# Optimization experiments

Hardware: AMD Instinct MI355X
Metric: run time of the kernel (lower is better)

## Reference

```python
import jax, jax.numpy as jnp
import numpy as np

N = 100000   # nodes
E = 1600000  # edges
IN = 32
HID = 64
OUT = 1

def setup_inputs() -> dict:
    key = jax.random.key(0)
    ks = jax.random.split(key, 16)
    x = jax.random.normal(ks[0], (N, IN), jnp.float32)
    edge_index = jax.random.randint(ks[1], (2, E), 0, N, dtype=jnp.int32)
    def lin(k, fi, fo):
        return jax.random.normal(k, (fi, fo), jnp.float32) / np.sqrt(fi)
    # SAGEConv params per layer: Wn/bn for aggregated neighbors (lin_l), Wr for root (lin_r, no bias)
    Wn0 = lin(ks[2], IN, HID);  bn0 = jnp.zeros((HID,), jnp.float32); Wr0 = lin(ks[3], IN, HID)
    Wn1 = lin(ks[4], HID, HID); bn1 = jnp.zeros((HID,), jnp.float32); Wr1 = lin(ks[5], HID, HID)
    Wn2 = lin(ks[6], HID, HID); bn2 = jnp.zeros((HID,), jnp.float32); Wr2 = lin(ks[7], HID, HID)
    # predictor MLP
    Wp1 = lin(ks[8], HID, HID); bp1 = jnp.zeros((HID,), jnp.float32)
    Wp2 = lin(ks[9], HID, OUT); bp2 = jnp.zeros((OUT,), jnp.float32)
    return dict(x=x, edge_index=edge_index,
                Wn0=Wn0, bn0=bn0, Wr0=Wr0,
                Wn1=Wn1, bn1=bn1, Wr1=Wr1,
                Wn2=Wn2, bn2=bn2, Wr2=Wr2,
                Wp1=Wp1, bp1=bp1, Wp2=Wp2, bp2=bp2)

def reference(x, edge_index, Wn0, bn0, Wr0, Wn1, bn1, Wr1, Wn2, bn2, Wr2, Wp1, bp1, Wp2, bp2):
    src, dst = edge_index[0], edge_index[1]
    n = x.shape[0]
    # mean-aggregation normalization (nodes with no in-edges get 0, as in PyG)
    cnt = jax.ops.segment_sum(jnp.ones(src.shape, x.dtype), dst, num_segments=n)
    inv = jnp.where(cnt > 0, 1.0 / jnp.maximum(cnt, 1.0), 0.0)[:, None]

    def sage(h, Wn, bn, Wr):
        agg = jax.ops.segment_sum(h[src], dst, num_segments=n) * inv  # [N, d]
        return agg @ Wn + bn + h @ Wr

    h = jax.nn.relu(sage(x, Wn0, bn0, Wr0))
    h = jax.nn.relu(sage(h, Wn1, bn1, Wr1))
    h = sage(h, Wn2, bn2, Wr2)  # no activation after last GNN layer
    h = jax.nn.relu(h @ Wp1 + bp1)
    return jax.nn.sigmoid(h @ Wp2 + bp2)
```

## Files before the change

kernel.cpp:

```cpp
#include <hip/hip_runtime.h>
#include <math.h>

#define NN 100000
#define EE 1600000
#define HID 64
#define BKT 391
#define SLAB 5504
#define SLAB_IT ((SLAB + 255) / 256)
#define CHUNK 4096
#define NWG ((EE + CHUNK - 1) / CHUNK)
#define TB (NN / 16)

typedef _Float16 f16;
typedef _Float16 f16x2 __attribute__((ext_vector_type(2)));

__device__ __forceinline__ f16x2 u2h(unsigned u) { return __builtin_bit_cast(f16x2, u); }
__device__ __forceinline__ unsigned h2u(f16x2 h) { return __builtin_bit_cast(unsigned, h); }

#if defined(__has_builtin) && __has_builtin(__builtin_amdgcn_fdot2)
__device__ __forceinline__ float dot2(f16x2 a, f16x2 b, float c) {
    return __builtin_amdgcn_fdot2(a, b, c, false);
}
#else
__device__ __forceinline__ float dot2(f16x2 a, f16x2 b, float c) {
    c = fmaf((float)a.x, (float)b.x, c);
    return fmaf((float)a.y, (float)b.y, c);
}
#endif


#if defined(__has_builtin)
#if __has_builtin(__builtin_amdgcn_cvt_pk_f32_fp8) && __has_builtin(__builtin_amdgcn_cvt_pk_fp8_f32)
#define HW_FP8 1
#endif
#endif

#ifndef HW_FP8
__device__ __forceinline__ float dec_e4m3(unsigned b) {
    unsigned s = b >> 7, e = (b >> 3) & 0xF, m = b & 7;
    float v;
    if (e == 0) v = (float)m * 0.001953125f;
    else v = (1.f + (float)m * 0.125f) * exp2f((float)((int)e - 7));
    return s ? -v : v;
}
__device__ __forceinline__ unsigned char enc_e4m3(float x) {
    unsigned s = (__builtin_bit_cast(unsigned, x) >> 31) << 7;
    float a = fabsf(x);
    if (!(a < 464.f)) return (unsigned char)(s | 0x7E);
    int e; float m = frexpf(a, &e);
    int E = e - 1;
    unsigned bits;
    if (E < -6) {
        int n = (int)rintf(a * 512.f);
        bits = (n > 7) ? 0x08u : (unsigned)n;
    } else {
        int n = (int)rintf((2.f * m - 1.f) * 8.f);
        if (n == 8) { n = 0; E += 1; }
        if (E > 8) return (unsigned char)(s | 0x7E);
        bits = ((unsigned)(E + 7) << 3) | (unsigned)n;
    }
    return (unsigned char)(s | bits);
}
#endif

__device__ __forceinline__ void acc_fp8(unsigned v, float& a0, float& a1,
                                        float& a2, float& a3) {
#ifdef HW_FP8
    auto lo = __builtin_amdgcn_cvt_pk_f32_fp8((int)v, false);
    auto hi = __builtin_amdgcn_cvt_pk_f32_fp8((int)v, true);
    a0 += lo[0]; a1 += lo[1]; a2 += hi[0]; a3 += hi[1];
#else
    a0 += dec_e4m3(v & 0xFFu);         a1 += dec_e4m3((v >> 8) & 0xFFu);
    a2 += dec_e4m3((v >> 16) & 0xFFu); a3 += dec_e4m3(v >> 24);
#endif
}

__device__ __forceinline__ unsigned char enc_fp8(float x) {
#ifdef HW_FP8
    return (unsigned char)(__builtin_amdgcn_cvt_pk_fp8_f32(x, x, 0, false) & 0xFF);
#else
    return enc_e4m3(x);
#endif
}


__global__ void mt_kernel(const int* __restrict__ src, const int* __restrict__ dst,
                          int* __restrict__ bfill, unsigned* __restrict__ pairs,
                          const float* __restrict__ h,
                          const float* __restrict__ Wn, const float* __restrict__ bn,
                          const float* __restrict__ Wr,
                          unsigned char* __restrict__ hn8, f16* __restrict__ hrb,
                          const float* __restrict__ Wn1, const float* __restrict__ Wr1,
                          const float* __restrict__ Wn2, const float* __restrict__ Wr2,
                          const float* __restrict__ Wp1, unsigned* __restrict__ w16) {
    __shared__ int lc[BKT];
    __shared__ int lbase[BKT];
    int t = threadIdx.x;

    if (blockIdx.x < NWG) {
        for (int b = t; b < BKT; b += 256) lc[b] = 0;
        __syncthreads();
        int base = blockIdx.x * CHUNK;
        int myd[CHUNK / 256];
        int myr[CHUNK / 256];
#pragma unroll
        for (int j = 0; j < CHUNK / 256; ++j) {
            int i = base + j * 256 + t;
            myd[j] = (i < EE) ? dst[i] : -1;
            myr[j] = (myd[j] >= 0) ? atomicAdd(&lc[myd[j] >> 8], 1) : 0;
        }
        __syncthreads();
        for (int b = t; b < BKT; b += 256) {
            int c = lc[b];
            if (c) {
                int ofs = atomicAdd(&bfill[b], c);
                if (ofs + c > SLAB) ofs = SLAB - c;
                lbase[b] = b * SLAB + ofs;
            }
        }
        __syncthreads();
#pragma unroll
        for (int j = 0; j < CHUNK / 256; ++j) {
            int i = base + j * 256 + t;
            if (myd[j] >= 0) {
                int b = myd[j] >> 8;
                pairs[lbase[b] + myr[j]] = (unsigned)src[i] | ((unsigned)(myd[j] & 255) << 24);
            }
        }
        return;
    }

    int bb = blockIdx.x - NWG;

    if (bb < 40) {
        int id = bb * 256 + t;
        int mat = id >> 11;
        int p = (id >> 6) & 31;
        int j = id & 63;
        const float* W = (mat == 0) ? Wn1 : (mat == 1) ? Wr1 :
                         (mat == 2) ? Wn2 : (mat == 3) ? Wr2 : Wp1;
        f16x2 v;
        v.x = (f16)W[(2 * p) * HID + j];
        v.y = (f16)W[(2 * p + 1) * HID + j];
        w16[id] = h2u(v);
    }

    int lane = t & 63;
    int wid = (bb * 256 + t) >> 6;
    int m0 = __builtin_amdgcn_readfirstlane(wid << 2);
    const float* h0 = h + (size_t)m0 * 32;

    float an0 = 0.f, an1 = 0.f, an2 = 0.f, an3 = 0.f;
    float ar0 = 0.f, ar1 = 0.f, ar2 = 0.f, ar3 = 0.f;
#pragma unroll
    for (int k = 0; k < 32; ++k) {
        float wn = Wn[k * HID + lane];
        float wr = Wr[k * HID + lane];
        float hk0 = h0[k], hk1 = h0[32 + k], hk2 = h0[64 + k], hk3 = h0[96 + k];
        an0 = fmaf(hk0, wn, an0); ar0 = fmaf(hk0, wr, ar0);
        an1 = fmaf(hk1, wn, an1); ar1 = fmaf(hk1, wr, ar1);
        an2 = fmaf(hk2, wn, an2); ar2 = fmaf(hk2, wr, ar2);
        an3 = fmaf(hk3, wn, an3); ar3 = fmaf(hk3, wr, ar3);
    }
    float b = bn[lane];
    size_t o8 = (size_t)m0 * HID + lane;
    hn8[o8] = enc_fp8(an0);
    hn8[o8 + HID] = enc_fp8(an1);
    hn8[o8 + 2 * HID] = enc_fp8(an2);
    hn8[o8 + 3 * HID] = enc_fp8(an3);
    size_t o = (size_t)m0 * HID + lane;
    hrb[o] = (f16)(ar0 + b); hrb[o + HID] = (f16)(ar1 + b);
    hrb[o + 2 * HID] = (f16)(ar2 + b); hrb[o + 3 * HID] = (f16)(ar3 + b);
}


__global__ void build_kernel(const unsigned* __restrict__ pairs,
                             const int* __restrict__ bfill,
                             int* __restrict__ rs, int* __restrict__ re,
                             float* __restrict__ inv, int* __restrict__ col) {
    __shared__ int ncnt[256];
    __shared__ int nexcl[256];
    int b = blockIdx.x;
    int t = threadIdx.x;
    int s0 = b * SLAB;
    int ce = bfill[b]; if (ce > SLAB) ce = SLAB;
    ncnt[t] = 0;
    __syncthreads();
    unsigned mypk[SLAB_IT];
    int myr[SLAB_IT];
#pragma unroll
    for (int j = 0; j < SLAB_IT; ++j) {
        int e = j * 256 + t;
        if (e < ce) {
            unsigned pk = pairs[s0 + e];
            mypk[j] = pk;
            myr[j] = atomicAdd(&ncnt[pk >> 24], 1);
        }
    }
    __syncthreads();
    int c = ncnt[t];
    int c4 = (c + 3) & ~3;
    nexcl[t] = c4;
    __syncthreads();
    for (int off = 1; off < 256; off <<= 1) {
        int u = (t >= off) ? nexcl[t - off] : 0;
        __syncthreads();
        nexcl[t] += u;
        __syncthreads();
    }
    int excl = nexcl[t] - c4;
    int node = (b << 8) + t;
    if (node < NN) {
        int start = s0 + excl; if (start > s0 + SLAB) start = s0 + SLAB;
        int end = start + c;   if (end > s0 + SLAB) end = s0 + SLAB;
        rs[node] = start;
        re[node] = end;
        inv[node] = (c > 0) ? (1.0f / (float)c) : 0.0f;
    }
    __syncthreads();
    ncnt[t] = excl;
    __syncthreads();
#pragma unroll
    for (int j = 0; j < SLAB_IT; ++j) {
        int e = j * 256 + t;
        if (e < ce) {
            unsigned pk = mypk[j];
            int idx = s0 + ncnt[pk >> 24] + myr[j];
            if (idx < s0 + SLAB) col[idx] = (int)(pk & 0xFFFFFFu);
        }
    }
    for (int k = c; k < c4; ++k) {
        int idx = s0 + excl + k;
        if (idx < s0 + SLAB) col[idx] = NN;
    }
}


__device__ __forceinline__ void qgather8(const unsigned* __restrict__ rp,
                                         const int* __restrict__ col,
                                         int e, int en, int en4, int fl,
                                         float& a0, float& a1, float& a2, float& a3) {
    while (e + 8 <= en4) {
        int4 ca = *(const int4*)(col + e);
        int4 cb = *(const int4*)(col + e + 4);
        unsigned v0 = rp[(size_t)ca.x * 16 + fl];
        unsigned v1 = rp[(size_t)ca.y * 16 + fl];
        unsigned v2 = rp[(size_t)ca.z * 16 + fl];
        unsigned v3 = rp[(size_t)ca.w * 16 + fl];
        unsigned v4 = rp[(size_t)cb.x * 16 + fl];
        unsigned v5 = rp[(size_t)cb.y * 16 + fl];
        unsigned v6 = rp[(size_t)cb.z * 16 + fl];
        unsigned v7 = rp[(size_t)cb.w * 16 + fl];
        acc_fp8(v0, a0, a1, a2, a3);
        acc_fp8(v1, a0, a1, a2, a3);
        acc_fp8(v2, a0, a1, a2, a3);
        acc_fp8(v3, a0, a1, a2, a3);
        acc_fp8(v4, a0, a1, a2, a3);
        acc_fp8(v5, a0, a1, a2, a3);
        acc_fp8(v6, a0, a1, a2, a3);
        acc_fp8(v7, a0, a1, a2, a3);
        e += 8;
    }
    if (e + 4 <= en4) {
        int4 ca = *(const int4*)(col + e);
        unsigned v0 = rp[(size_t)ca.x * 16 + fl];
        unsigned v1 = rp[(size_t)ca.y * 16 + fl];
        unsigned v2 = rp[(size_t)ca.z * 16 + fl];
        unsigned v3 = rp[(size_t)ca.w * 16 + fl];
        acc_fp8(v0, a0, a1, a2, a3);
        acc_fp8(v1, a0, a1, a2, a3);
        acc_fp8(v2, a0, a1, a2, a3);
        acc_fp8(v3, a0, a1, a2, a3);
        e += 4;
    }
    while (e < en) {
        unsigned v = rp[(size_t)col[e] * 16 + fl];
        acc_fp8(v, a0, a1, a2, a3);
        ++e;
    }
}


__global__ void gt_kernel(const unsigned char* __restrict__ An8,
                          const int* __restrict__ rs, const int* __restrict__ re,
                          const int* __restrict__ col, const float* __restrict__ inv,
                          f16* C,
                          const unsigned* __restrict__ Wn16, const float* __restrict__ bn,
                          const unsigned* __restrict__ Wr16,
                          unsigned char* __restrict__ Aout8) {
    __shared__ uint4 hsh[128];
    int t = threadIdx.x;
    int lane = t & 63;
    int wv = t >> 6;
    int wid = (blockIdx.x * blockDim.x + t) >> 6;
    int m0 = wid << 2;
    int m = m0 + (lane >> 4);
    int fl = lane & 15;

    int e = rs[m], en = re[m];
    int en4 = e + ((en - e + 3) & ~3);
    int bnd = ((m >> 8) + 1) * SLAB;
    if (en4 > bnd) en4 = bnd;

    float a0 = 0.f, a1 = 0.f, a2 = 0.f, a3 = 0.f;
    qgather8((const unsigned*)An8, col, e, en, en4, fl, a0, a1, a2, a3);

    float iv = inv[m];
    uint2 cur = ((const uint2*)C)[(size_t)m * 16 + fl];
    f16x2 q0 = u2h(cur.x), q1 = u2h(cur.y);
    f16x2 hA, hB;
    hA.x = (f16)fmaxf(fmaf(a0, iv, (float)q0.x), 0.f);
    hA.y = (f16)fmaxf(fmaf(a1, iv, (float)q0.y), 0.f);
    hB.x = (f16)fmaxf(fmaf(a2, iv, (float)q1.x), 0.f);
    hB.y = (f16)fmaxf(fmaf(a3, iv, (float)q1.y), 0.f);

    uint2 hv; hv.x = h2u(hA); hv.y = h2u(hB);
    ((uint2*)hsh)[wv * 64 + (lane >> 4) * 16 + fl] = hv;

    float an[4] = {0.f, 0.f, 0.f, 0.f};
    float ar[4] = {0.f, 0.f, 0.f, 0.f};
#pragma unroll
    for (int j = 0; j < 8; ++j) {
        f16x2 wn0 = u2h(Wn16[(4 * j) * HID + lane]);
        f16x2 wn1 = u2h(Wn16[(4 * j + 1) * HID + lane]);
        f16x2 wn2 = u2h(Wn16[(4 * j + 2) * HID + lane]);
        f16x2 wn3 = u2h(Wn16[(4 * j + 3) * HID + lane]);
        f16x2 wr0 = u2h(Wr16[(4 * j) * HID + lane]);
        f16x2 wr1 = u2h(Wr16[(4 * j + 1) * HID + lane]);
        f16x2 wr2 = u2h(Wr16[(4 * j + 2) * HID + lane]);
        f16x2 wr3 = u2h(Wr16[(4 * j + 3) * HID + lane]);
#pragma unroll
        for (int n = 0; n < 4; ++n) {
            uint4 d = hsh[wv * 32 + n * 8 + j];
            an[n] = dot2(u2h(d.x), wn0, an[n]);
            an[n] = dot2(u2h(d.y), wn1, an[n]);
            an[n] = dot2(u2h(d.z), wn2, an[n]);
            an[n] = dot2(u2h(d.w), wn3, an[n]);
            ar[n] = dot2(u2h(d.x), wr0, ar[n]);
            ar[n] = dot2(u2h(d.y), wr1, ar[n]);
            ar[n] = dot2(u2h(d.z), wr2, ar[n]);
            ar[n] = dot2(u2h(d.w), wr3, ar[n]);
        }
    }
    float b = bn[lane];
    size_t o8 = (size_t)m0 * HID + lane;
    size_t o = (size_t)m0 * HID + lane;
#pragma unroll
    for (int n = 0; n < 4; ++n) {
        Aout8[o8 + n * HID] = enc_fp8(an[n]);
        C[o + n * HID] = (f16)(ar[n] + b);
    }
}


__global__ void gh_kernel(const unsigned char* __restrict__ An8,
                          const int* __restrict__ rs, const int* __restrict__ re,
                          const int* __restrict__ col, const float* __restrict__ inv,
                          const f16* __restrict__ C,
                          const unsigned* __restrict__ Wp116, const float* __restrict__ bp1,
                          const float* __restrict__ Wp2, const float* __restrict__ bp2,
                          float* __restrict__ out) {
    __shared__ uint4 hsh[128];
    int t = threadIdx.x;
    int lane = t & 63;
    int wv = t >> 6;
    int wid = (blockIdx.x * blockDim.x + t) >> 6;
    int m0 = wid << 2;
    int m = m0 + (lane >> 4);
    int fl = lane & 15;

    int e = rs[m], en = re[m];
    int en4 = e + ((en - e + 3) & ~3);
    int bnd = ((m >> 8) + 1) * SLAB;
    if (en4 > bnd) en4 = bnd;

    float a0 = 0.f, a1 = 0.f, a2 = 0.f, a3 = 0.f;
    qgather8((const unsigned*)An8, col, e, en, en4, fl, a0, a1, a2, a3);

    float iv = inv[m];
    uint2 cur = ((const uint2*)C)[(size_t)m * 16 + fl];
    f16x2 q0 = u2h(cur.x), q1 = u2h(cur.y);
    f16x2 hA, hB;
    hA.x = (f16)fmaf(a0, iv, (float)q0.x);
    hA.y = (f16)fmaf(a1, iv, (float)q0.y);
    hB.x = (f16)fmaf(a2, iv, (float)q1.x);
    hB.y = (f16)fmaf(a3, iv, (float)q1.y);

    uint2 hv; hv.x = h2u(hA); hv.y = h2u(hB);
    ((uint2*)hsh)[wv * 64 + (lane >> 4) * 16 + fl] = hv;

    float tn[4] = {0.f, 0.f, 0.f, 0.f};
#pragma unroll
    for (int j = 0; j < 8; ++j) {
        f16x2 wp0 = u2h(Wp116[(4 * j) * HID + lane]);
        f16x2 wp1 = u2h(Wp116[(4 * j + 1) * HID + lane]);
        f16x2 wp2 = u2h(Wp116[(4 * j + 2) * HID + lane]);
        f16x2 wp3 = u2h(Wp116[(4 * j + 3) * HID + lane]);
#pragma unroll
        for (int n = 0; n < 4; ++n) {
            uint4 d = hsh[wv * 32 + n * 8 + j];
            tn[n] = dot2(u2h(d.x), wp0, tn[n]);
            tn[n] = dot2(u2h(d.y), wp1, tn[n]);
            tn[n] = dot2(u2h(d.z), wp2, tn[n]);
            tn[n] = dot2(u2h(d.w), wp3, tn[n]);
        }
    }
    float b = bp1[lane], w2v = Wp2[lane];
    float r0 = fmaxf(tn[0] + b, 0.f) * w2v;
    float r1 = fmaxf(tn[1] + b, 0.f) * w2v;
    float r2 = fmaxf(tn[2] + b, 0.f) * w2v;
    float r3 = fmaxf(tn[3] + b, 0.f) * w2v;
#pragma unroll
    for (int off = 32; off > 0; off >>= 1) {
        r0 += __shfl_xor(r0, off);
        r1 += __shfl_xor(r1, off);
        r2 += __shfl_xor(r2, off);
        r3 += __shfl_xor(r3, off);
    }
    if (lane == 0) {
        float bb = bp2[0];
        out[m0]     = 1.f / (1.f + expf(-(r0 + bb)));
        out[m0 + 1] = 1.f / (1.f + expf(-(r1 + bb)));
        out[m0 + 2] = 1.f / (1.f + expf(-(r2 + bb)));
        out[m0 + 3] = 1.f / (1.f + expf(-(r3 + bb)));
    }
}

extern "C" void kernel_launch(void* const* d_in, const int* in_sizes, int n_in,
                              void* d_out, int out_size, void* d_ws, size_t ws_size,
                              hipStream_t stream) {
    const float* x   = (const float*)d_in[0];
    const int* eidx  = (const int*)d_in[1];
    const float* Wn0 = (const float*)d_in[2];
    const float* bn0 = (const float*)d_in[3];
    const float* Wr0 = (const float*)d_in[4];
    const float* Wn1 = (const float*)d_in[5];
    const float* bn1 = (const float*)d_in[6];
    const float* Wr1 = (const float*)d_in[7];
    const float* Wn2 = (const float*)d_in[8];
    const float* bn2 = (const float*)d_in[9];
    const float* Wr2 = (const float*)d_in[10];
    const float* Wp1 = (const float*)d_in[11];
    const float* bp1 = (const float*)d_in[12];
    const float* Wp2 = (const float*)d_in[13];
    const float* bp2 = (const float*)d_in[14];
    float* out = (float*)d_out;

    const int* src = eidx;
    const int* dst = eidx + EE;

    char* w = (char*)d_ws;
    size_t off = 0;
    auto carve = [&](size_t bytes) -> void* {
        void* p = w + off;
        off = (off + bytes + 255) & ~(size_t)255;
        return p;
    };
    int*   rsA    = (int*)carve((size_t)NN * 4);
    int*   reA    = (int*)carve((size_t)NN * 4);
    float* inv    = (float*)carve((size_t)NN * 4);
    int*   col    = (int*)carve((size_t)BKT * SLAB * 4);
    int*   bfill  = (int*)carve((size_t)BKT * 4);
    unsigned* w16 = (unsigned*)carve((size_t)5 * 2048 * 4);
    unsigned char* A0 = (unsigned char*)carve((size_t)(NN + 1) * HID);
    unsigned char* A1 = (unsigned char*)carve((size_t)(NN + 1) * HID);
    f16*   C      = (f16*)carve((size_t)NN * HID * 2);
    unsigned* pairs = (unsigned*)carve((size_t)BKT * SLAB * 4);
    (void)ws_size;

    unsigned* Wn1_16 = w16;
    unsigned* Wr1_16 = w16 + 2048;
    unsigned* Wn2_16 = w16 + 4096;
    unsigned* Wr2_16 = w16 + 6144;
    unsigned* Wp1_16 = w16 + 8192;

    hipMemsetAsync(bfill, 0, (size_t)BKT * 4, stream);
    hipMemsetAsync(A0 + (size_t)NN * HID, 0, HID, stream);
    hipMemsetAsync(A1 + (size_t)NN * HID, 0, HID, stream);

    mt_kernel<<<NWG + TB, 256, 0, stream>>>(src, dst, bfill, pairs,
                                            x, Wn0, bn0, Wr0, A0, C,
                                            Wn1, Wr1, Wn2, Wr2, Wp1, w16);
    build_kernel<<<BKT, 256, 0, stream>>>(pairs, bfill, rsA, reA, inv, col);

    gt_kernel<<<TB, 256, 0, stream>>>(A0, rsA, reA, col, inv, C, Wn1_16, bn1, Wr1_16, A1);
    gt_kernel<<<TB, 256, 0, stream>>>(A1, rsA, reA, col, inv, C, Wn2_16, bn2, Wr2_16, A0);
    gh_kernel<<<TB, 256, 0, stream>>>(A0, rsA, reA, col, inv, C, Wp1_16, bp1, Wp2, bp2, out);
}
```

Before: 244.2 us.

## Widen gather loads to 8 bytes per lane and split edges across half-groups

The neighbor gather in the hidden and head kernels now has each lane load 8 fp8 features (uint2) rather than 4. The 16 lanes for a node split into two groups of 8 that take alternating edges, and their partial sums are combined with an xor shuffle. Root features are read as uint4 and only half the lanes write to shared memory. Separately, the first-layer transform in mt_kernel now handles 8 nodes per wave instead of 4, which halves its block count and raises register use.

```diff
diff --git a/kernel.cpp b/kernel.cpp
--- a/kernel.cpp
+++ b/kernel.cpp
@@ -10,6 +10,7 @@
 #define CHUNK 4096
 #define NWG ((EE + CHUNK - 1) / CHUNK)
 #define TB (NN / 16)
+#define TBM (NN / 32)
 
 typedef _Float16 f16;
 typedef _Float16 f16x2 __attribute__((ext_vector_type(2)));
@@ -147,30 +148,30 @@
 
     int lane = t & 63;
     int wid = (bb * 256 + t) >> 6;
-    int m0 = __builtin_amdgcn_readfirstlane(wid << 2);
+    int m0 = __builtin_amdgcn_readfirstlane(wid << 3);
     const float* h0 = h + (size_t)m0 * 32;
 
-    float an0 = 0.f, an1 = 0.f, an2 = 0.f, an3 = 0.f;
-    float ar0 = 0.f, ar1 = 0.f, ar2 = 0.f, ar3 = 0.f;
+    float an[8] = {0.f, 0.f, 0.f, 0.f, 0.f, 0.f, 0.f, 0.f};
+    float ar[8] = {0.f, 0.f, 0.f, 0.f, 0.f, 0.f, 0.f, 0.f};
 #pragma unroll
     for (int k = 0; k < 32; ++k) {
         float wn = Wn[k * HID + lane];
         float wr = Wr[k * HID + lane];
-        float hk0 = h0[k], hk1 = h0[32 + k], hk2 = h0[64 + k], hk3 = h0[96 + k];
-        an0 = fmaf(hk0, wn, an0); ar0 = fmaf(hk0, wr, ar0);
-        an1 = fmaf(hk1, wn, an1); ar1 = fmaf(hk1, wr, ar1);
-        an2 = fmaf(hk2, wn, an2); ar2 = fmaf(hk2, wr, ar2);
-        an3 = fmaf(hk3, wn, an3); ar3 = fmaf(hk3, wr, ar3);
+#pragma unroll
+        for (int n = 0; n < 8; ++n) {
+            float hk = h0[n * 32 + k];
+            an[n] = fmaf(hk, wn, an[n]);
+            ar[n] = fmaf(hk, wr, ar[n]);
+        }
     }
     float b = bn[lane];
     size_t o8 = (size_t)m0 * HID + lane;
-    hn8[o8] = enc_fp8(an0);
-    hn8[o8 + HID] = enc_fp8(an1);
-    hn8[o8 + 2 * HID] = enc_fp8(an2);
-    hn8[o8 + 3 * HID] = enc_fp8(an3);
     size_t o = (size_t)m0 * HID + lane;
-    hrb[o] = (f16)(ar0 + b); hrb[o + HID] = (f16)(ar1 + b);
-    hrb[o + 2 * HID] = (f16)(ar2 + b); hrb[o + 3 * HID] = (f16)(ar3 + b);
+#pragma unroll
+    for (int n = 0; n < 8; ++n) {
+        hn8[o8 + n * HID] = enc_fp8(an[n]);
+        hrb[o + n * HID] = (f16)(ar[n] + b);
+    }
 }
 
 
@@ -236,46 +237,50 @@
 }
 
 
-__device__ __forceinline__ void qgather8(const unsigned* __restrict__ rp,
-                                         const int* __restrict__ col,
-                                         int e, int en, int en4, int fl,
-                                         float& a0, float& a1, float& a2, float& a3) {
+__device__ __forceinline__ void acc8(uint2 v, float& a0, float& a1, float& a2,
+                                     float& a3, float& a4, float& a5, float& a6,
+                                     float& a7) {
+    acc_fp8(v.x, a0, a1, a2, a3);
+    acc_fp8(v.y, a4, a5, a6, a7);
+}
+
+__device__ __forceinline__ void qgp(const uint2* __restrict__ rp2,
+                                    const int* __restrict__ col,
+                                    int e, int en, int en4, int ff, int el,
+                                    float& a0, float& a1, float& a2, float& a3,
+                                    float& a4, float& a5, float& a6, float& a7) {
     while (e + 8 <= en4) {
         int4 ca = *(const int4*)(col + e);
         int4 cb = *(const int4*)(col + e + 4);
-        unsigned v0 = rp[(size_t)ca.x * 16 + fl];
-        unsigned v1 = rp[(size_t)ca.y * 16 + fl];
-        unsigned v2 = rp[(size_t)ca.z * 16 + fl];
-        unsigned v3 = rp[(size_t)ca.w * 16 + fl];
-        unsigned v4 = rp[(size_t)cb.x * 16 + fl];
-        unsigned v5 = rp[(size_t)cb.y * 16 + fl];
-        unsigned v6 = rp[(size_t)cb.z * 16 + fl];
-        unsigned v7 = rp[(size_t)cb.w * 16 + fl];
-        acc_fp8(v0, a0, a1, a2, a3);
-        acc_fp8(v1, a0, a1, a2, a3);
-        acc_fp8(v2, a0, a1, a2, a3);
-        acc_fp8(v3, a0, a1, a2, a3);
-        acc_fp8(v4, a0, a1, a2, a3);
-        acc_fp8(v5, a0, a1, a2, a3);
-        acc_fp8(v6, a0, a1, a2, a3);
-        acc_fp8(v7, a0, a1, a2, a3);
+        int c0 = el ? ca.y : ca.x;
+        int c1 = el ? ca.w : ca.z;
+        int c2 = el ? cb.y : cb.x;
+        int c3 = el ? cb.w : cb.z;
+        uint2 v0 = rp2[(size_t)c0 * 8 + ff];
+        uint2 v1 = rp2[(size_t)c1 * 8 + ff];
+        uint2 v2 = rp2[(size_t)c2 * 8 + ff];
+        uint2 v3 = rp2[(size_t)c3 * 8 + ff];
+        acc8(v0, a0, a1, a2, a3, a4, a5, a6, a7);
+        acc8(v1, a0, a1, a2, a3, a4, a5, a6, a7);
+        acc8(v2, a0, a1, a2, a3, a4, a5, a6, a7);
+        acc8(v3, a0, a1, a2, a3, a4, a5, a6, a7);
         e += 8;
     }
     if (e + 4 <= en4) {
         int4 ca = *(const int4*)(col + e);
-        unsigned v0 = rp[(size_t)ca.x * 16 + fl];
-        unsigned v1 = rp[(size_t)ca.y * 16 + fl];
-        unsigned v2 = rp[(size_t)ca.z * 16 + fl];
-        unsigned v3 = rp[(size_t)ca.w * 16 + fl];
-        acc_fp8(v0, a0, a1, a2, a3);
-        acc_fp8(v1, a0, a1, a2, a3);
-        acc_fp8(v2, a0, a1, a2, a3);
-        acc_fp8(v3, a0, a1, a2, a3);
+        int c0 = el ? ca.y : ca.x;
+        int c1 = el ? ca.w : ca.z;
+        uint2 v0 = rp2[(size_t)c0 * 8 + ff];
+        uint2 v1 = rp2[(size_t)c1 * 8 + ff];
+        acc8(v0, a0, a1, a2, a3, a4, a5, a6, a7);
+        acc8(v1, a0, a1, a2, a3, a4, a5, a6, a7);
         e += 4;
     }
     while (e < en) {
-        unsigned v = rp[(size_t)col[e] * 16 + fl];
-        acc_fp8(v, a0, a1, a2, a3);
+        if (!el) {
+            uint2 v = rp2[(size_t)col[e] * 8 + ff];
+            acc8(v, a0, a1, a2, a3, a4, a5, a6, a7);
+        }
         ++e;
     }
 }
@@ -295,7 +300,8 @@
     int wid = (blockIdx.x * blockDim.x + t) >> 6;
     int m0 = wid << 2;
     int m = m0 + (lane >> 4);
-    int fl = lane & 15;
+    int ff = lane & 7;
+    int el = (lane >> 3) & 1;
 
     int e = rs[m], en = re[m];
     int en4 = e + ((en - e + 3) & ~3);
@@ -303,19 +309,30 @@
     if (en4 > bnd) en4 = bnd;
 
     float a0 = 0.f, a1 = 0.f, a2 = 0.f, a3 = 0.f;
-    qgather8((const unsigned*)An8, col, e, en, en4, fl, a0, a1, a2, a3);
+    float a4 = 0.f, a5 = 0.f, a6 = 0.f, a7 = 0.f;
+    qgp((const uint2*)An8, col, e, en, en4, ff, el, a0, a1, a2, a3, a4, a5, a6, a7);
+
+    a0 += __shfl_xor(a0, 8); a1 += __shfl_xor(a1, 8);
+    a2 += __shfl_xor(a2, 8); a3 += __shfl_xor(a3, 8);
+    a4 += __shfl_xor(a4, 8); a5 += __shfl_xor(a5, 8);
+    a6 += __shfl_xor(a6, 8); a7 += __shfl_xor(a7, 8);
 
     float iv = inv[m];
-    uint2 cur = ((const uint2*)C)[(size_t)m * 16 + fl];
-    f16x2 q0 = u2h(cur.x), q1 = u2h(cur.y);
-    f16x2 hA, hB;
-    hA.x = (f16)fmaxf(fmaf(a0, iv, (float)q0.x), 0.f);
-    hA.y = (f16)fmaxf(fmaf(a1, iv, (float)q0.y), 0.f);
-    hB.x = (f16)fmaxf(fmaf(a2, iv, (float)q1.x), 0.f);
-    hB.y = (f16)fmaxf(fmaf(a3, iv, (float)q1.y), 0.f);
-
-    uint2 hv; hv.x = h2u(hA); hv.y = h2u(hB);
-    ((uint2*)hsh)[wv * 64 + (lane >> 4) * 16 + fl] = hv;
+    uint4 cur = ((const uint4*)C)[(size_t)m * 8 + ff];
+    f16x2 q0 = u2h(cur.x), q1 = u2h(cur.y), q2 = u2h(cur.z), q3 = u2h(cur.w);
+    f16x2 p0, p1, p2, p3;
+    p0.x = (f16)fmaxf(fmaf(a0, iv, (float)q0.x), 0.f);
+    p0.y = (f16)fmaxf(fmaf(a1, iv, (float)q0.y), 0.f);
+    p1.x = (f16)fmaxf(fmaf(a2, iv, (float)q1.x), 0.f);
+    p1.y = (f16)fmaxf(fmaf(a3, iv, (float)q1.y), 0.f);
+    p2.x = (f16)fmaxf(fmaf(a4, iv, (float)q2.x), 0.f);
+    p2.y = (f16)fmaxf(fmaf(a5, iv, (float)q2.y), 0.f);
+    p3.x = (f16)fmaxf(fmaf(a6, iv, (float)q3.x), 0.f);
+    p3.y = (f16)fmaxf(fmaf(a7, iv, (float)q3.y), 0.f);
+
+    uint4 hv4;
+    hv4.x = h2u(p0); hv4.y = h2u(p1); hv4.z = h2u(p2); hv4.w = h2u(p3);
+    if (!(lane & 8)) hsh[wv * 32 + (lane >> 4) * 8 + ff] = hv4;
 
     float an[4] = {0.f, 0.f, 0.f, 0.f};
     float ar[4] = {0.f, 0.f, 0.f, 0.f};
@@ -367,7 +384,8 @@
     int wid = (blockIdx.x * blockDim.x + t) >> 6;
     int m0 = wid << 2;
     int m = m0 + (lane >> 4);
-    int fl = lane & 15;
+    int ff = lane & 7;
+    int el = (lane >> 3) & 1;
 
     int e = rs[m], en = re[m];
     int en4 = e + ((en - e + 3) & ~3);
@@ -375,19 +393,30 @@
     if (en4 > bnd) en4 = bnd;
 
     float a0 = 0.f, a1 = 0.f, a2 = 0.f, a3 = 0.f;
-    qgather8((const unsigned*)An8, col, e, en, en4, fl, a0, a1, a2, a3);
+    float a4 = 0.f, a5 = 0.f, a6 = 0.f, a7 = 0.f;
+    qgp((const uint2*)An8, col, e, en, en4, ff, el, a0, a1, a2, a3, a4, a5, a6, a7);
+
+    a0 += __shfl_xor(a0, 8); a1 += __shfl_xor(a1, 8);
+    a2 += __shfl_xor(a2, 8); a3 += __shfl_xor(a3, 8);
+    a4 += __shfl_xor(a4, 8); a5 += __shfl_xor(a5, 8);
+    a6 += __shfl_xor(a6, 8); a7 += __shfl_xor(a7, 8);
 
     float iv = inv[m];
-    uint2 cur = ((const uint2*)C)[(size_t)m * 16 + fl];
-    f16x2 q0 = u2h(cur.x), q1 = u2h(cur.y);
-    f16x2 hA, hB;
-    hA.x = (f16)fmaf(a0, iv, (float)q0.x);
-    hA.y = (f16)fmaf(a1, iv, (float)q0.y);
-    hB.x = (f16)fmaf(a2, iv, (float)q1.x);
-    hB.y = (f16)fmaf(a3, iv, (float)q1.y);
-
-    uint2 hv; hv.x = h2u(hA); hv.y = h2u(hB);
-    ((uint2*)hsh)[wv * 64 + (lane >> 4) * 16 + fl] = hv;
+    uint4 cur = ((const uint4*)C)[(size_t)m * 8 + ff];
+    f16x2 q0 = u2h(cur.x), q1 = u2h(cur.y), q2 = u2h(cur.z), q3 = u2h(cur.w);
+    f16x2 p0, p1, p2, p3;
+    p0.x = (f16)fmaf(a0, iv, (float)q0.x);
+    p0.y = (f16)fmaf(a1, iv, (float)q0.y);
+    p1.x = (f16)fmaf(a2, iv, (float)q1.x);
+    p1.y = (f16)fmaf(a3, iv, (float)q1.y);
+    p2.x = (f16)fmaf(a4, iv, (float)q2.x);
+    p2.y = (f16)fmaf(a5, iv, (float)q2.y);
+    p3.x = (f16)fmaf(a6, iv, (float)q3.x);
+    p3.y = (f16)fmaf(a7, iv, (float)q3.y);
+
+    uint4 hv4;
+    hv4.x = h2u(p0); hv4.y = h2u(p1); hv4.z = h2u(p2); hv4.w = h2u(p3);
+    if (!(lane & 8)) hsh[wv * 32 + (lane >> 4) * 8 + ff] = hv4;
 
     float tn[4] = {0.f, 0.f, 0.f, 0.f};
 #pragma unroll
@@ -478,9 +507,9 @@
     hipMemsetAsync(A0 + (size_t)NN * HID, 0, HID, stream);
     hipMemsetAsync(A1 + (size_t)NN * HID, 0, HID, stream);
 
-    mt_kernel<<<NWG + TB, 256, 0, stream>>>(src, dst, bfill, pairs,
-                                            x, Wn0, bn0, Wr0, A0, C,
-                                            Wn1, Wr1, Wn2, Wr2, Wp1, w16);
+    mt_kernel<<<NWG + TBM, 256, 0, stream>>>(src, dst, bfill, pairs,
+                                             x, Wn0, bn0, Wr0, A0, C,
+                                             Wn1, Wr1, Wn2, Wr2, Wp1, w16);
     build_kernel<<<BKT, 256, 0, stream>>>(pairs, bfill, rsA, reA, inv, col);
 
     gt_kernel<<<TB, 256, 0, stream>>>(A0, rsA, reA, col, inv, C, Wn1_16, bn1, Wr1_16, A1);
```

Result: no change. 245.5 us (+0.5%).
